# Optimization experiments

Hardware: AMD Instinct MI355X
Metric: run time of the kernel (lower is better)

## Reference

```python
import jax, jax.numpy as jnp
import numpy as np

_DIR_INLIER = 0.9          # _HOUGHVOTING_DIRECTION_INLIER
_NUM_INLIER = 500          # _HOUGHVOTING_NUM_INLIER
_LABEL_THRESH = 500        # _LABEL2MASK_THRESHOL
NUM_CLASSES = 10
BS, H, W = 1, 240, 320


def setup_inputs() -> dict:
    key = jax.random.key(0)
    k_lab, k_cx, k_cy, k_nx, k_ny, k_nd = jax.random.split(key, 6)
    label = jax.random.randint(k_lab, (BS, H, W), 0, NUM_CLASSES + 1).astype(jnp.int32)
    xs = jnp.arange(W, dtype=jnp.float32)
    ys = jnp.arange(H, dtype=jnp.float32)
    xv, yv = jnp.meshgrid(xs, ys)  # [H, W] each
    # per-class ground-truth centers well inside the image so voting converges
    cxs = jax.random.uniform(k_cx, (NUM_CLASSES,), minval=40.0, maxval=W - 40.0)
    cys = jax.random.uniform(k_cy, (NUM_CLASSES,), minval=40.0, maxval=H - 40.0)
    dx = cxs[:, None, None] - xv[None]  # [C, H, W]
    dy = cys[:, None, None] - yv[None]
    nrm = jnp.sqrt(dx * dx + dy * dy) + 1e-6
    dirx = dx / nrm + 0.01 * jax.random.normal(k_nx, (NUM_CLASSES, H, W))
    diry = dy / nrm + 0.01 * jax.random.normal(k_ny, (NUM_CLASSES, H, W))
    depth = (1.0 + 0.3 * jnp.arange(NUM_CLASSES, dtype=jnp.float32))[:, None, None] \
        + 0.01 * jax.random.normal(k_nd, (NUM_CLASSES, H, W))
    cmap = jnp.stack([dirx, diry, depth], axis=1).reshape(3 * NUM_CLASSES, H, W)
    centermap = jnp.broadcast_to(cmap[None], (BS, 3 * NUM_CLASSES, H, W)).astype(jnp.float32)
    return {"label": label, "centermap": centermap}


def hough_voting(label, centermap, num_classes):
    bs, H_, W_ = label.shape
    xs = jnp.arange(W_, dtype=jnp.float32)
    ys = jnp.arange(H_, dtype=jnp.float32)
    xv, yv = jnp.meshgrid(xs, ys)            # [H, W]
    xsi = jnp.arange(W_, dtype=jnp.int32)
    all_centers, all_depths = [], []
    for b in range(bs):
        lab = label[b]
        row_c, row_d = [], []
        for cls in range(1, num_classes + 1):
            cmask = lab == cls                                    # [H, W]
            enough = cmask.sum() >= _LABEL_THRESH
            c3 = centermap[b, (cls - 1) * 3:(cls - 1) * 3 + 3]    # [3, H, W]
            slope = c3[1] / c3[0]                                  # dy/dx per pixel
            # every masked pixel votes along its line at every column x
            y_idx = jnp.round(yv[:, :, None] + slope[:, :, None] * (xs[None, None, :] - xv[:, :, None])).astype(jnp.int32)  # [H, W, W]
            valid = (y_idx >= 0) & (y_idx < H_) & cmask[:, :, None]
            bins = jnp.clip(y_idx, 0, H_ - 1) * W_ + xsi[None, None, :]
            hist = jnp.zeros(H_ * W_, jnp.float32).at[bins.ravel()].add(valid.ravel().astype(jnp.float32))
            cbin = jnp.argmax(hist)
            inlier_num = hist[cbin]
            cx = (cbin % W_).astype(jnp.float32)
            cy = (cbin // W_).astype(jnp.float32)
            # depth: mean of depth channel over direction-consistent class pixels
            disx = xv - cx
            disy = yv - cy
            dnrm = jnp.sqrt(disx * disx + disy * disy)
            dot = jnp.abs((disx / dnrm) * c3[0] + (disy / dnrm) * c3[1])  # nan at center -> compares False, as torch
            imask = (dot >= _DIR_INLIER) & cmask
            cnt = imask.sum().astype(jnp.float32)
            dsum = jnp.sum(jnp.where(imask, c3[2], 0.0))
            dmean = jnp.where(cnt > 0, dsum / jnp.maximum(cnt, 1.0), jnp.nan)
            trig = enough & (inlier_num > _NUM_INLIER)
            row_c.append(jnp.where(trig, jnp.stack([cx, cy]), jnp.zeros(2, jnp.float32)))
            row_d.append(jnp.where(trig, dmean, 0.0))
        all_centers.append(jnp.stack(row_c))
        all_depths.append(jnp.stack(row_d))
    return jnp.stack(all_centers), jnp.stack(all_depths)


def reference(label, centermap):
    return hough_voting(label, centermap, NUM_CLASSES)
```

## Files before the change

### kernel.cpp

```cpp
#include <hip/hip_runtime.h>
#include <stdint.h>

#define H 240
#define W 320
#define NPIX (H * W)
#define NCLS 10
#define COLS 4
#define BIN_BITS 20
#define BIN_MASK 0xFFFFFu


__global__ void k_init(uint32_t* ws) {
    int i = threadIdx.x;
    if (i < 128) ws[i] = 0;
}

__global__ __launch_bounds__(256) void k_compact(const int* __restrict__ label,
                                                 const float* __restrict__ cm,
                                                 uint32_t* __restrict__ cls_cnt,
                                                 uint2* __restrict__ list) {
    __shared__ uint32_t lcnt[NCLS];
    __shared__ uint32_t lbase[NCLS];
    int p = blockIdx.x * 256 + threadIdx.x;
    if (threadIdx.x < NCLS) lcnt[threadIdx.x] = 0;
    __syncthreads();

    int l = label[p];
    bool match = (l >= 1 && l <= NCLS);
    int cls = l - 1;
    uint32_t li = 0;
    if (match) li = atomicAdd(&lcnt[cls], 1u);
    __syncthreads();

    if (threadIdx.x < NCLS) {
        uint32_t c = lcnt[threadIdx.x];
        lbase[threadIdx.x] = c ? atomicAdd(&cls_cnt[threadIdx.x], c) : 0u;
    }
    __syncthreads();

    if (match) {
        float dirx = cm[(cls * 3 + 0) * NPIX + p];
        float diry = cm[(cls * 3 + 1) * NPIX + p];
        float slope = diry / dirx;
        int y = p / W, x = p - y * W;
        uint2 e;
        e.x = (uint32_t)(x | (y << 16));
        e.y = __float_as_uint(slope);
        list[cls * NPIX + lbase[cls] + li] = e;
    }
}

__global__ __launch_bounds__(256) void k_vote(const uint32_t* __restrict__ cls_cnt,
                                              const uint2* __restrict__ list,
                                              unsigned long long* __restrict__ best) {
    int cls = blockIdx.y;
    int x0 = blockIdx.x * COLS;
    __shared__ uint32_t hist[COLS][H];
    __shared__ unsigned long long wred[4];
    for (int i = threadIdx.x; i < COLS * H; i += 256) ((uint32_t*)hist)[i] = 0;
    __syncthreads();

    int n = (int)cls_cnt[cls];
    const uint2* lst = list + cls * NPIX;
    for (int i0 = 0; i0 < n; i0 += 256) {
        int i = i0 + (int)threadIdx.x;
        bool inb = (i < n);
        uint2 e;
        e.x = 0u; e.y = 0u;
        if (inb) e = lst[i];
        float slope = __uint_as_float(e.y);
        float xf = (float)(e.x & 0xFFFFu);
        float yf = (float)(e.x >> 16);
#pragma unroll
        for (int c = 0; c < COLS; ++c) {
            float dx = (float)(x0 + c) - xf;
            float r = rintf(yf + slope * dx);
            bool valid = inb && (r >= 0.0f) && (r <= (float)(H - 1));
            int bin = (int)r;
            unsigned long long vm = __ballot(valid);
            if (vm != 0ull) {
                int src = __ffsll((unsigned long long)vm) - 1;
                int b0 = __shfl(bin, src);
                unsigned long long sm = __ballot(!valid || bin == b0);
                if (sm == ~0ull) {
                    if ((int)(threadIdx.x & 63u) == src)
                        atomicAdd(&hist[c][b0], (uint32_t)__popcll(vm));
                } else if (valid) {
                    atomicAdd(&hist[c][bin], 1u);
                }
            }
        }
    }
    __syncthreads();

    unsigned long long k = 0;
    for (int i = threadIdx.x; i < COLS * H; i += 256) {
        int c = i / H, y = i - c * H;
        uint32_t v = hist[c][y];
        uint32_t bin = (uint32_t)(y * W + x0 + c);
        unsigned long long key =
            ((unsigned long long)v << BIN_BITS) | (unsigned long long)(BIN_MASK - bin);
        if (key > k) k = key;
    }
#pragma unroll
    for (int off = 32; off > 0; off >>= 1) {
        unsigned long long o = __shfl_down(k, off);
        if (o > k) k = o;
    }
    if ((threadIdx.x & 63u) == 0u) wred[threadIdx.x >> 6] = k;
    __syncthreads();
    if (threadIdx.x == 0) {
        unsigned long long kk = wred[0];
#pragma unroll
        for (int w = 1; w < 4; ++w) if (wred[w] > kk) kk = wred[w];
        atomicMax(&best[cls], kk);
    }
}

__global__ __launch_bounds__(256) void k_inlier_final(
    const int* __restrict__ label, const float* __restrict__ cm,
    const uint32_t* __restrict__ cls_cnt,
    const unsigned long long* __restrict__ best,
    uint32_t* __restrict__ icnt, float* __restrict__ dsum,
    uint32_t* __restrict__ done, float* __restrict__ out) {
    __shared__ float scx[NCLS], scy[NCLS];
    __shared__ uint32_t scnt[NCLS];
    __shared__ float ssum[NCLS];
    __shared__ int slast;
    int tid = threadIdx.x;
    if (tid < NCLS) {
        unsigned long long key = best[tid];
        uint32_t bin = BIN_MASK - (uint32_t)(key & BIN_MASK);
        scx[tid] = (float)(bin % W);
        scy[tid] = (float)(bin / W);
        scnt[tid] = 0u;
        ssum[tid] = 0.0f;
    }
    __syncthreads();

    int p = blockIdx.x * 256 + tid;
    int l = label[p];
    if (l >= 1 && l <= NCLS) {
        int cls = l - 1;
        int y = p / W, x = p - y * W;
        float disx = (float)x - scx[cls];
        float disy = (float)y - scy[cls];
        float dn = sqrtf(disx * disx + disy * disy);
        if (dn > 0.0f) {
            float c0 = cm[(cls * 3 + 0) * NPIX + p];
            float c1 = cm[(cls * 3 + 1) * NPIX + p];
            float dot = fabsf((disx / dn) * c0 + (disy / dn) * c1);
            if (dot >= 0.9f) {
                atomicAdd(&scnt[cls], 1u);
                atomicAdd(&ssum[cls], cm[(cls * 3 + 2) * NPIX + p]);
            }
        }
    }
    __syncthreads();

    if (tid < NCLS) {
        if (scnt[tid]) atomicAdd(&icnt[tid], scnt[tid]);
        if (ssum[tid] != 0.0f) atomicAdd(&dsum[tid], ssum[tid]);
    }
    if (tid == 0) {
        __threadfence();
        uint32_t d = atomicAdd(done, 1u);
        slast = (d == (uint32_t)(gridDim.x - 1)) ? 1 : 0;
    }
    __syncthreads();

    if (slast && tid < NCLS) {
        uint32_t tc = atomicAdd(&icnt[tid], 0u);
        float td = atomicAdd(&dsum[tid], 0.0f);
        unsigned long long key = best[tid];
        uint32_t hv = (uint32_t)(key >> BIN_BITS);
        bool trig = (cls_cnt[tid] >= 500u) && (hv > 500u);
        float c = (float)tc;
        float dm = (c > 0.0f) ? (td / fmaxf(c, 1.0f)) : __builtin_nanf("");
        out[tid * 2 + 0] = trig ? scx[tid] : 0.0f;
        out[tid * 2 + 1] = trig ? scy[tid] : 0.0f;
        out[2 * NCLS + tid] = trig ? dm : 0.0f;
    }
}

extern "C" void kernel_launch(void* const* d_in, const int* in_sizes, int n_in,
                              void* d_out, int out_size, void* d_ws, size_t ws_size,
                              hipStream_t stream) {
    const int* label = (const int*)d_in[0];
    const float* cm = (const float*)d_in[1];
    float* out = (float*)d_out;
    char* ws = (char*)d_ws;

    uint32_t* cls_cnt = (uint32_t*)(ws + 0);
    unsigned long long* best = (unsigned long long*)(ws + 64);
    uint32_t* icnt = (uint32_t*)(ws + 192);
    float* dsum = (float*)(ws + 256);
    uint32_t* done = (uint32_t*)(ws + 320);
    uint2* list = (uint2*)(ws + 512);

    k_init<<<1, 128, 0, stream>>>((uint32_t*)ws);
    k_compact<<<NPIX / 256, 256, 0, stream>>>(label, cm, cls_cnt, list);
    k_vote<<<dim3(W / COLS, NCLS), 256, 0, stream>>>(cls_cnt, list, best);
    k_inlier_final<<<NPIX / 256, 256, 0, stream>>>(label, cm, cls_cnt, best,
                                                   icnt, dsum, done, out);
}
```

Measured before the change: 107.9 us.

## Restructure voting so each wave lane handles one column of a 16-wide tile

The vote kernel now gives each block a 16-column tile and 1024 threads. Each lane is mapped to one column and one of four pixels per wave, and the histogram is padded to reduce LDS bank conflicts. This replaces the per-column ballot/shuffle aggregation with direct LDS atomics. Each list entry is now read by 16 lanes instead of being re-read by 80 blocks, so global traffic drops fourfold, but the grid shrinks to 200 blocks and there are more atomic collisions within a wave.

New measurement: 114.6 us. 6.2% more time.

```diff
diff --git a/kernel.cpp b/kernel.cpp
--- a/kernel.cpp
+++ b/kernel.cpp
@@ -5,7 +5,8 @@
 #define W 320
 #define NPIX (H * W)
 #define NCLS 10
-#define COLS 4
+#define TILE 16
+#define HPAD 241
 #define BIN_BITS 20
 #define BIN_MASK 0xFFFFFu
 
@@ -50,53 +51,37 @@
     }
 }
 
-__global__ __launch_bounds__(256) void k_vote(const uint32_t* __restrict__ cls_cnt,
-                                              const uint2* __restrict__ list,
-                                              unsigned long long* __restrict__ best) {
+__global__ __launch_bounds__(1024) void k_vote(const uint32_t* __restrict__ cls_cnt,
+                                               const uint2* __restrict__ list,
+                                               unsigned long long* __restrict__ best) {
     int cls = blockIdx.y;
-    int x0 = blockIdx.x * COLS;
-    __shared__ uint32_t hist[COLS][H];
-    __shared__ unsigned long long wred[4];
-    for (int i = threadIdx.x; i < COLS * H; i += 256) ((uint32_t*)hist)[i] = 0;
+    int x0 = blockIdx.x * TILE;
+    __shared__ uint32_t hist[TILE * HPAD];
+    __shared__ unsigned long long wred[16];
+    int tid = threadIdx.x;
+    for (int i = tid; i < TILE * HPAD; i += 1024) hist[i] = 0;
     __syncthreads();
 
     int n = (int)cls_cnt[cls];
     const uint2* lst = list + cls * NPIX;
-    for (int i0 = 0; i0 < n; i0 += 256) {
-        int i = i0 + (int)threadIdx.x;
-        bool inb = (i < n);
-        uint2 e;
-        e.x = 0u; e.y = 0u;
-        if (inb) e = lst[i];
+    int wave = tid >> 6, lane = tid & 63;
+    int g = lane >> 4, cit = lane & 15;
+    float colf = (float)(x0 + cit);
+    uint32_t* hcol = &hist[cit * HPAD];
+    for (int i = wave * 4 + g; i < n; i += 64) {
+        uint2 e = lst[i];
         float slope = __uint_as_float(e.y);
         float xf = (float)(e.x & 0xFFFFu);
         float yf = (float)(e.x >> 16);
-#pragma unroll
-        for (int c = 0; c < COLS; ++c) {
-            float dx = (float)(x0 + c) - xf;
-            float r = rintf(yf + slope * dx);
-            bool valid = inb && (r >= 0.0f) && (r <= (float)(H - 1));
-            int bin = (int)r;
-            unsigned long long vm = __ballot(valid);
-            if (vm != 0ull) {
-                int src = __ffsll((unsigned long long)vm) - 1;
-                int b0 = __shfl(bin, src);
-                unsigned long long sm = __ballot(!valid || bin == b0);
-                if (sm == ~0ull) {
-                    if ((int)(threadIdx.x & 63u) == src)
-                        atomicAdd(&hist[c][b0], (uint32_t)__popcll(vm));
-                } else if (valid) {
-                    atomicAdd(&hist[c][bin], 1u);
-                }
-            }
-        }
+        float r = rintf(yf + slope * (colf - xf));
+        if (r >= 0.0f && r <= 239.0f) atomicAdd(&hcol[(int)r], 1u);
     }
     __syncthreads();
 
     unsigned long long k = 0;
-    for (int i = threadIdx.x; i < COLS * H; i += 256) {
+    for (int i = tid; i < TILE * H; i += 1024) {
         int c = i / H, y = i - c * H;
-        uint32_t v = hist[c][y];
+        uint32_t v = hist[c * HPAD + y];
         uint32_t bin = (uint32_t)(y * W + x0 + c);
         unsigned long long key =
             ((unsigned long long)v << BIN_BITS) | (unsigned long long)(BIN_MASK - bin);
@@ -107,12 +92,12 @@
         unsigned long long o = __shfl_down(k, off);
         if (o > k) k = o;
     }
-    if ((threadIdx.x & 63u) == 0u) wred[threadIdx.x >> 6] = k;
+    if (lane == 0) wred[wave] = k;
     __syncthreads();
-    if (threadIdx.x == 0) {
+    if (tid == 0) {
         unsigned long long kk = wred[0];
 #pragma unroll
-        for (int w = 1; w < 4; ++w) if (wred[w] > kk) kk = wred[w];
+        for (int w = 1; w < 16; ++w) if (wred[w] > kk) kk = wred[w];
         atomicMax(&best[cls], kk);
     }
 }
@@ -200,7 +185,7 @@
 
     k_init<<<1, 128, 0, stream>>>((uint32_t*)ws);
     k_compact<<<NPIX / 256, 256, 0, stream>>>(label, cm, cls_cnt, list);
-    k_vote<<<dim3(W / COLS, NCLS), 256, 0, stream>>>(cls_cnt, list, best);
+    k_vote<<<dim3(W / TILE, NCLS), 1024, 0, stream>>>(cls_cnt, list, best);
     k_inlier_final<<<NPIX / 256, 256, 0, stream>>>(label, cm, cls_cnt, best,
                                                    icnt, dsum, done, out);
 }
```
